# Kernel tuning notes

Measured on AMD Instinct MI355X. Metric: run time of the kernel, lower is better.

Reference implementation:

```python
import jax, jax.numpy as jnp
import numpy as np

HIDDEN = 768
NUM_HEADS = 12
HEAD_SIZE = HIDDEN // NUM_HEADS
LN_EPS = 1e-12


def setup_inputs() -> dict:
    key = jax.random.key(0)
    ks = jax.random.split(key, 10)
    B, S, H = 32, 512, HIDDEN
    std = 1.0 / np.sqrt(H)
    inp = {
        "x": jax.random.normal(ks[0], (B, S, H), dtype=jnp.float32),
        "additive_attention_mask": jnp.zeros((B, 1, 1, S), dtype=jnp.float32),
        "Wq": jax.random.normal(ks[1], (H, H), dtype=jnp.float32) * std,
        "bq": jax.random.normal(ks[2], (H,), dtype=jnp.float32) * 0.02,
        "Wk": jax.random.normal(ks[3], (H, H), dtype=jnp.float32) * std,
        "bk": jax.random.normal(ks[4], (H,), dtype=jnp.float32) * 0.02,
        "Wv": jax.random.normal(ks[5], (H, H), dtype=jnp.float32) * std,
        "bv": jax.random.normal(ks[6], (H,), dtype=jnp.float32) * 0.02,
        "Wo": jax.random.normal(ks[7], (H, H), dtype=jnp.float32) * std,
        "bo": jax.random.normal(ks[8], (H,), dtype=jnp.float32) * 0.02,
        "ln_w": jnp.ones((H,), dtype=jnp.float32),
        "ln_b": jnp.zeros((H,), dtype=jnp.float32),
    }
    return inp


def _split_heads(y):
    # (b, s, h) -> (b, n_heads, s, head_size)
    b, s, _ = y.shape
    return y.reshape(b, s, NUM_HEADS, HEAD_SIZE).transpose(0, 2, 1, 3)


def reference(x, additive_attention_mask, Wq, bq, Wk, bk, Wv, bv, Wo, bo, ln_w, ln_b):
    # Linear projections (torch Linear: x @ W.T + b)
    q = _split_heads(x @ Wq.T + bq)  # b n s d
    k = _split_heads(x @ Wk.T + bk)
    v = _split_heads(x @ Wv.T + bv)

    scores = jnp.einsum("bnqd,bnkd->bnqk", q, k) / np.sqrt(HEAD_SIZE)
    scores = scores + additive_attention_mask  # (b,1,1,s) broadcasts
    attn = jax.nn.softmax(scores, axis=-1)

    weighted = jnp.einsum("bnqk,bnkd->bnqd", attn, v)
    b, n, s, d = weighted.shape
    weighted = weighted.transpose(0, 2, 1, 3).reshape(b, s, n * d)
    attn_out = weighted @ Wo.T + bo

    # residual + LayerNorm (dropout is identity in eval)
    y = x + attn_out
    mean = jnp.mean(y, axis=-1, keepdims=True)
    var = jnp.var(y, axis=-1, keepdims=True)
    y = (y - mean) / jnp.sqrt(var + LN_EPS)
    return y * ln_w + ln_b
```

## Files before the change

### kernel.cpp

```cpp
#include <hip/hip_runtime.h>

#define HIDDEN 768
#define NHEAD 12
#define HDIM 64
#define SEQ 512
#define BATCH 32
#define MTOT (BATCH*SEQ)

typedef __attribute__((ext_vector_type(8))) short short8;
typedef __attribute__((ext_vector_type(4))) float f32x4;
typedef __attribute__((ext_vector_type(4))) unsigned short us4;

#define LOG2E 1.44269504088896340736f

__device__ __forceinline__ unsigned short f2bf(float f){
  unsigned u = __builtin_bit_cast(unsigned, f);
  u += 0x7fff + ((u >> 16) & 1);
  return (unsigned short)(u >> 16);
}

__device__ __forceinline__ float bf2f(unsigned short s){
  unsigned u = ((unsigned)s) << 16;
  return __builtin_bit_cast(float, u);
}

__device__ __forceinline__ float fexp2(float x){
  float r;
  asm("v_exp_f32 %0, %1\n\ts_nop 0" : "=v"(r) : "v"(x));
  return r;
}

__device__ __forceinline__ void gload16(unsigned short* lds, const unsigned short* g){
  __builtin_amdgcn_global_load_lds(
      (const __attribute__((address_space(1))) void*)g,
      (__attribute__((address_space(3))) void*)lds, 16, 0, 0);
}

__global__ __launch_bounds__(256) void cvt_kernel(const float* __restrict__ in,
                                                  unsigned short* __restrict__ out, int n4){
  int i = blockIdx.x * blockDim.x + threadIdx.x;
  if (i >= n4) return;
  float4 v = ((const float4*)in)[i];
  ushort4 o;
  o.x = f2bf(v.x); o.y = f2bf(v.y); o.z = f2bf(v.z); o.w = f2bf(v.w);
  ((ushort4*)out)[i] = o;
}

__global__ __launch_bounds__(256) void cvt4_kernel(
    const float* __restrict__ w0, const float* __restrict__ w1,
    const float* __restrict__ w2, const float* __restrict__ w3,
    unsigned short* __restrict__ o0, unsigned short* __restrict__ o1,
    unsigned short* __restrict__ o2, unsigned short* __restrict__ o3){
  const int which = blockIdx.y;
  const float* in = (which==0)?w0:((which==1)?w1:((which==2)?w2:w3));
  unsigned short* out = (which==0)?o0:((which==1)?o1:((which==2)?o2:o3));
  int i = blockIdx.x * blockDim.x + threadIdx.x;
  float4 v = ((const float4*)in)[i];
  ushort4 o;
  o.x = f2bf(v.x); o.y = f2bf(v.y); o.z = f2bf(v.z); o.w = f2bf(v.w);
  ((ushort4*)out)[i] = o;
}

#define STAGE_A(buf, kt_) do { \
    const int kc_ = (kt_)*64; \
    gload16(&sA[buf][(size_t)(tid)*8],      gA + kc_); \
    gload16(&sA[buf][(size_t)(512+tid)*8],  gA + (size_t)64*HIDDEN + kc_); \
    gload16(&sA[buf][(size_t)(1024+tid)*8], gA + (size_t)128*HIDDEN + kc_); \
    gload16(&sA[buf][(size_t)(1536+tid)*8], gA + (size_t)192*HIDDEN + kc_); \
  } while(0)

#define STAGE_B(buf, kt_) do { \
    const int kc_ = (kt_)*64; \
    gload16(&sB[buf][(size_t)(tid)*8],      gB + kc_); \
    gload16(&sB[buf][(size_t)(512+tid)*8],  gB + (size_t)64*HIDDEN + kc_); \
    gload16(&sB[buf][(size_t)(1024+tid)*8], gB + (size_t)128*HIDDEN + kc_); \
  } while(0)

#define GEMM8_MAIN() \
  STAGE_A(0, 0); STAGE_B(0, 0); \
  for (int kt = 0; kt < 12; ++kt) { \
    const int c = kt & 1; \
    asm volatile("s_waitcnt vmcnt(0)" ::: "memory"); \
    __builtin_amdgcn_s_barrier(); \
    __builtin_amdgcn_sched_barrier(0); \
    const unsigned short* bA = sA[c]; \
    const unsigned short* bB = sB[c]; \
    short8 bf0[3], bf1[3]; \
    _Pragma("unroll") \
    for (int q = 0; q < 4; ++q) { \
      if (kt < 11) { \
        if (q == 0) STAGE_A(c^1, kt+1); \
        else if (q == 1) STAGE_B(c^1, kt+1); \
      } \
      short8 a00 = *(const short8*)&bA[aoff[q*2]]; \
      short8 a01 = *(const short8*)&bA[aoff[q*2] ^ 32]; \
      short8 a10 = *(const short8*)&bA[aoff[q*2+1]]; \
      short8 a11 = *(const short8*)&bA[aoff[q*2+1] ^ 32]; \
      if (q == 0) { \
        _Pragma("unroll") \
        for (int i = 0; i < 3; i++){ \
          bf0[i] = *(const short8*)&bB[boff[i]]; \
          bf1[i] = *(const short8*)&bB[boff[i] ^ 32]; \
        } \
      } \
      asm volatile("s_waitcnt lgkmcnt(0)" ::: "memory"); \
      __builtin_amdgcn_sched_barrier(0); \
      __builtin_amdgcn_s_setprio(1); \
      _Pragma("unroll") \
      for (int ni = 0; ni < 3; ni++){ \
        acc[q*2][ni]   = __builtin_amdgcn_mfma_f32_16x16x32_bf16(a00, bf0[ni], acc[q*2][ni], 0, 0, 0); \
        acc[q*2][ni]   = __builtin_amdgcn_mfma_f32_16x16x32_bf16(a01, bf1[ni], acc[q*2][ni], 0, 0, 0); \
        acc[q*2+1][ni] = __builtin_amdgcn_mfma_f32_16x16x32_bf16(a10, bf0[ni], acc[q*2+1][ni], 0, 0, 0); \
        acc[q*2+1][ni] = __builtin_amdgcn_mfma_f32_16x16x32_bf16(a11, bf1[ni], acc[q*2+1][ni], 0, 0, 0); \
      } \
      __builtin_amdgcn_s_setprio(0); \
      __builtin_amdgcn_sched_barrier(0); \
      __builtin_amdgcn_s_barrier(); \
    } \
  }

__global__ __launch_bounds__(512, 2) void qkv_gemm(
    const unsigned short* __restrict__ A,
    const unsigned short* __restrict__ Wq,
    const unsigned short* __restrict__ Wk,
    const unsigned short* __restrict__ Wv,
    const float* __restrict__ bq,
    const float* __restrict__ bk,
    const float* __restrict__ bv,
    unsigned short* __restrict__ Qo,
    unsigned short* __restrict__ Ko,
    unsigned short* __restrict__ VTo)
{
  __shared__ unsigned short sA[2][16384];
  __shared__ unsigned short sB[2][12288];

  const int flat = blockIdx.x;
  const int swzb = (flat & 7) * 96 + (flat >> 3);
  const int mi_ = swzb / 12;
  const int rem = swzb % 12;
  const int mode = rem >> 2;
  const int n0 = (rem & 3) * 192;
  const int m0 = mi_ * 256;
  const unsigned short* W = (mode==0) ? Wq : ((mode==1) ? Wk : Wv);
  const float* bias = (mode==0) ? bq : ((mode==1) ? bk : bv);

  const int tid = threadIdx.x;
  const int lane = tid & 63;
  const int wid = tid >> 6;
  const int wm = wid >> 2, wn = wid & 3;
  const int g = lane >> 4, l16 = lane & 15;

  const int rS = tid >> 3;
  const int gc = (tid & 7) ^ (rS & 7);
  const unsigned short* gA = &A[(size_t)(m0 + rS)*HIDDEN + gc*8];
  const unsigned short* gB = &W[(size_t)(n0 + rS)*HIDDEN + gc*8];

  int aoff[8], boff[3];
  #pragma unroll
  for (int i = 0; i < 8; i++){
    int rm = wm*128 + i*16 + l16;
    aoff[i] = rm*64 + ((g ^ (rm&7)) * 8);
  }
  #pragma unroll
  for (int i = 0; i < 3; i++){
    int rn = wn*48 + i*16 + l16;
    boff[i] = rn*64 + ((g ^ (rn&7)) * 8);
  }

  f32x4 acc[8][3];
  #pragma unroll
  for (int i = 0; i < 8; i++)
    #pragma unroll
    for (int j = 0; j < 3; j++) acc[i][j] = (f32x4){0.f,0.f,0.f,0.f};

  GEMM8_MAIN();

  float bvv[3];
  #pragma unroll
  for (int ni = 0; ni < 3; ni++) bvv[ni] = bias[n0 + wn*48 + ni*16 + l16];
  #pragma unroll
  for (int mi2 = 0; mi2 < 8; mi2++) {
    int mbase = m0 + wm*128 + mi2*16 + g*4;
    int b = mbase >> 9, s = mbase & 511;
    #pragma unroll
    for (int ni = 0; ni < 3; ni++) {
      int ncol = n0 + wn*48 + ni*16 + l16;
      int h = ncol >> 6, d = ncol & 63;
      if (mode == 2) {
        us4 v;
        #pragma unroll
        for (int r = 0; r < 4; r++) v[r] = f2bf(acc[mi2][ni][r] + bvv[ni]);
        *(us4*)&VTo[(((size_t)(b*NHEAD)+h)*HDIM + d)*SEQ + s] = v;
      } else {
        #pragma unroll
        for (int r = 0; r < 4; r++) {
          float val = acc[mi2][ni][r] + bvv[ni];
          if (mode == 0) Qo[(((size_t)(b*NHEAD)+h)*SEQ + s + r)*HDIM + d] = f2bf(val * 0.1803368801f);
          else           Ko[(((size_t)(b*NHEAD)+h)*SEQ + s + r)*HDIM + d] = f2bf(val);
        }
      }
    }
  }
}

__global__ __launch_bounds__(512, 2) void proj_gemm(
    const unsigned short* __restrict__ A,
    const unsigned short* __restrict__ W,
    const float* __restrict__ bias,
    unsigned short* __restrict__ Out)
{
  __shared__ unsigned short sA[2][16384];
  __shared__ unsigned short sB[2][12288];

  const int flat = blockIdx.x;
  const int swzb = (flat & 7) * 32 + (flat >> 3);
  const int m0 = (swzb >> 2) * 256;
  const int n0 = (swzb & 3) * 192;

  const int tid = threadIdx.x;
  const int lane = tid & 63;
  const int wid = tid >> 6;
  const int wm = wid >> 2, wn = wid & 3;
  const int g = lane >> 4, l16 = lane & 15;

  const int rS = tid >> 3;
  const int gc = (tid & 7) ^ (rS & 7);
  const unsigned short* gA = &A[(size_t)(m0 + rS)*HIDDEN + gc*8];
  const unsigned short* gB = &W[(size_t)(n0 + rS)*HIDDEN + gc*8];

  int aoff[8], boff[3];
  #pragma unroll
  for (int i = 0; i < 8; i++){
    int rm = wm*128 + i*16 + l16;
    aoff[i] = rm*64 + ((g ^ (rm&7)) * 8);
  }
  #pragma unroll
  for (int i = 0; i < 3; i++){
    int rn = wn*48 + i*16 + l16;
    boff[i] = rn*64 + ((g ^ (rn&7)) * 8);
  }

  f32x4 acc[8][3];
  #pragma unroll
  for (int i = 0; i < 8; i++)
    #pragma unroll
    for (int j = 0; j < 3; j++) acc[i][j] = (f32x4){0.f,0.f,0.f,0.f};

  GEMM8_MAIN();

  float bvv[3];
  #pragma unroll
  for (int ni = 0; ni < 3; ni++) bvv[ni] = bias[n0 + wn*48 + ni*16 + l16];
  #pragma unroll
  for (int mi2 = 0; mi2 < 8; mi2++) {
    int mbase = m0 + wm*128 + mi2*16 + g*4;
    #pragma unroll
    for (int ni = 0; ni < 3; ni++) {
      int ncol = n0 + wn*48 + ni*16 + l16;
      #pragma unroll
      for (int r = 0; r < 4; r++)
        Out[(size_t)(mbase + r)*HIDDEN + ncol] = f2bf(acc[mi2][ni][r] + bvv[ni]);
    }
  }
}

__global__ __launch_bounds__(256) void attn_kernel(
    const unsigned short* __restrict__ Q,
    const unsigned short* __restrict__ K,
    const unsigned short* __restrict__ VT,
    const float* __restrict__ mask,
    unsigned short* __restrict__ ctx)
{
  __shared__ unsigned short sK[3][4096];
  __shared__ unsigned short sV[3][4096];
  __shared__ unsigned short P_lds[4*16*68];
  __shared__ float sMask[512];

  const int flat = blockIdx.x;
  const int swzb = (flat & 7) * 192 + (flat >> 3);
  const int qt = swzb & 3;
  const int bh = swzb >> 2;
  const int b = bh / NHEAD, h = bh % NHEAD;
  const int tid = threadIdx.x;
  const int lane = tid & 63;
  const int wid = tid >> 6;
  const int g = lane >> 4, l16 = lane & 15;
  const int qbase = qt*128 + wid*32;

  const int rS = tid >> 3;
  const int cbS = (tid & 7) ^ (rS & 7);
  const size_t khb = (size_t)bh * SEQ;
  const unsigned short* gK  = &K[(khb + rS)*HDIM + cbS*8];
  const unsigned short* gK2 = gK + (size_t)32*HDIM;
  const unsigned short* gV  = &VT[((size_t)bh*HDIM + rS)*SEQ + cbS*8];
  const unsigned short* gV2 = gV + (size_t)32*SEQ;

  sMask[tid]       = mask[b*SEQ + tid] * LOG2E;
  sMask[tid + 256] = mask[b*SEQ + tid + 256] * LOG2E;

  short8 aQ0[2], aQ1[2];
  #pragma unroll
  for (int q16 = 0; q16 < 2; q16++){
    const unsigned short* qp = &Q[(khb + qbase + q16*16 + l16)*HDIM];
    aQ0[q16] = *(const short8*)&qp[g*8];
    aQ1[q16] = *(const short8*)&qp[32 + g*8];
  }

  int off[4];
  {
    const int sw = (g ^ (l16 & 7)) * 8;
    #pragma unroll
    for (int i = 0; i < 4; i++) off[i] = (i*16 + l16)*64 + sw;
  }

  float l_r[2][4];
  f32x4 o_acc[2][4];
  #pragma unroll
  for (int q16 = 0; q16 < 2; q16++){
    #pragma unroll
    for (int r = 0; r < 4; r++) l_r[q16][r] = 0.f;
    #pragma unroll
    for (int dt = 0; dt < 4; dt++) o_acc[q16][dt] = (f32x4){0.f,0.f,0.f,0.f};
  }

#define KSTAGE(buf_, t_) do { \
    gload16(&sK[buf_][wid*512],        gK  + (size_t)(t_)*64*HDIM); \
    gload16(&sK[buf_][2048 + wid*512], gK2 + (size_t)(t_)*64*HDIM); \
    gload16(&sV[buf_][wid*512],        gV  + (t_)*64); \
    gload16(&sV[buf_][2048 + wid*512], gV2 + (t_)*64); \
  } while(0)

  KSTAGE(0, 0);
  KSTAGE(1, 1);
  asm volatile("s_waitcnt lgkmcnt(0)" ::: "memory");

  int cb = 0;
  for (int kt = 0; kt < 8; ++kt) {
    if (kt < 7) asm volatile("s_waitcnt vmcnt(4)" ::: "memory");
    else        asm volatile("s_waitcnt vmcnt(0)" ::: "memory");
    __builtin_amdgcn_s_barrier();
    __builtin_amdgcn_sched_barrier(0);
    if (kt < 6) { const int sb = (cb == 0) ? 2 : cb - 1; KSTAGE(sb, kt + 2); }
    const unsigned short* bK = sK[cb];
    const unsigned short* bV = sV[cb];
    const int kv0 = kt * 64;

    f32x4 sacc[2][4];
    #pragma unroll
    for (int ct = 0; ct < 4; ++ct) {
      short8 k0 = *(const short8*)&bK[off[ct]];
      short8 k1 = *(const short8*)&bK[off[ct] ^ 32];
      f32x4 s0 = (f32x4){0.f,0.f,0.f,0.f}, s1 = (f32x4){0.f,0.f,0.f,0.f};
      __builtin_amdgcn_s_setprio(1);
      s0 = __builtin_amdgcn_mfma_f32_16x16x32_bf16(aQ0[0], k0, s0, 0, 0, 0);
      s0 = __builtin_amdgcn_mfma_f32_16x16x32_bf16(aQ1[0], k1, s0, 0, 0, 0);
      s1 = __builtin_amdgcn_mfma_f32_16x16x32_bf16(aQ0[1], k0, s1, 0, 0, 0);
      s1 = __builtin_amdgcn_mfma_f32_16x16x32_bf16(aQ1[1], k1, s1, 0, 0, 0);
      __builtin_amdgcn_s_setprio(0);
      float mv = sMask[kv0 + ct*16 + l16];
      sacc[0][ct] = s0 + mv;
      sacc[1][ct] = s1 + mv;
    }

    #pragma unroll
    for (int q16 = 0; q16 < 2; q16++){
      #pragma unroll
      for (int ct = 0; ct < 4; ct++){
        #pragma unroll
        for (int r = 0; r < 4; r++){
          float p = fexp2(sacc[q16][ct][r]);
          l_r[q16][r] += p;
          P_lds[(wid*16 + g*4 + r)*68 + ct*16 + l16] =
              (unsigned short)(__builtin_bit_cast(unsigned, p) >> 16);
        }
      }
      asm volatile("s_waitcnt lgkmcnt(0)" ::: "memory");
      __builtin_amdgcn_sched_barrier(0);
      short8 pa0 = *(const short8*)&P_lds[(wid*16 + l16)*68 + g*8];
      short8 pa1 = *(const short8*)&P_lds[(wid*16 + l16)*68 + 32 + g*8];
      __builtin_amdgcn_s_setprio(1);
      #pragma unroll
      for (int dt = 0; dt < 4; dt++){
        short8 v0 = *(const short8*)&bV[off[dt]];
        short8 v1 = *(const short8*)&bV[off[dt] ^ 32];
        o_acc[q16][dt] = __builtin_amdgcn_mfma_f32_16x16x32_bf16(pa0, v0, o_acc[q16][dt], 0, 0, 0);
        o_acc[q16][dt] = __builtin_amdgcn_mfma_f32_16x16x32_bf16(pa1, v1, o_acc[q16][dt], 0, 0, 0);
      }
      __builtin_amdgcn_s_setprio(0);
    }
    cb = (cb == 2) ? 0 : cb + 1;
  }

  #pragma unroll
  for (int q16 = 0; q16 < 2; q16++){
    #pragma unroll
    for (int o = 1; o <= 8; o <<= 1){
      #pragma unroll
      for (int r = 0; r < 4; r++) l_r[q16][r] += __shfl_xor(l_r[q16][r], o);
    }
    float inv[4];
    #pragma unroll
    for (int r = 0; r < 4; r++) inv[r] = 1.f / l_r[q16][r];
    #pragma unroll
    for (int dt = 0; dt < 4; dt++){
      #pragma unroll
      for (int r = 0; r < 4; r++){
        int s = qbase + q16*16 + g*4 + r;
        ctx[((size_t)(b*SEQ + s))*HIDDEN + h*HDIM + dt*16 + l16] = f2bf(o_acc[q16][dt][r] * inv[r]);
      }
    }
  }
#undef KSTAGE
}

__global__ __launch_bounds__(256) void resid_ln(
    const unsigned short* __restrict__ xb, const unsigned short* __restrict__ ao,
    const float* __restrict__ lnw, const float* __restrict__ lnb,
    float* __restrict__ out)
{
  const int row = blockIdx.x*4 + (threadIdx.x >> 6);
  const int lane = threadIdx.x & 63;
  const ushort4* xr = (const ushort4*)&xb[(size_t)row*HIDDEN];
  const ushort4* ar = (const ushort4*)&ao[(size_t)row*HIDDEN];
  float4 y[3];
  float s1 = 0.f, s2 = 0.f;
  #pragma unroll
  for (int j = 0; j < 3; j++){
    ushort4 xv = xr[lane + j*64];
    ushort4 av = ar[lane + j*64];
    float4 v;
    v.x = bf2f(xv.x) + bf2f(av.x); v.y = bf2f(xv.y) + bf2f(av.y);
    v.z = bf2f(xv.z) + bf2f(av.z); v.w = bf2f(xv.w) + bf2f(av.w);
    y[j] = v;
    s1 += v.x + v.y + v.z + v.w;
    s2 += v.x*v.x + v.y*v.y + v.z*v.z + v.w*v.w;
  }
  #pragma unroll
  for (int o = 1; o <= 32; o <<= 1){
    s1 += __shfl_xor(s1, o);
    s2 += __shfl_xor(s2, o);
  }
  float mean = s1 * (1.f/768.f);
  float var = s2 * (1.f/768.f) - mean*mean;
  float rstd = rsqrtf(var + 1e-12f);
  float4* orow = (float4*)&out[(size_t)row*HIDDEN];
  #pragma unroll
  for (int j = 0; j < 3; j++){
    float4 gm = ((const float4*)lnw)[lane + j*64];
    float4 bt = ((const float4*)lnb)[lane + j*64];
    float4 o;
    o.x = (y[j].x - mean)*rstd*gm.x + bt.x;
    o.y = (y[j].y - mean)*rstd*gm.y + bt.y;
    o.z = (y[j].z - mean)*rstd*gm.z + bt.z;
    o.w = (y[j].w - mean)*rstd*gm.w + bt.w;
    orow[lane + j*64] = o;
  }
}

extern "C" void kernel_launch(void* const* d_in, const int* in_sizes, int n_in,
                              void* d_out, int out_size, void* d_ws, size_t ws_size,
                              hipStream_t stream) {
  (void)in_sizes; (void)n_in; (void)out_size; (void)ws_size;
  const float* x    = (const float*)d_in[0];
  const float* mask = (const float*)d_in[1];
  const float* Wq   = (const float*)d_in[2];
  const float* bq   = (const float*)d_in[3];
  const float* Wk   = (const float*)d_in[4];
  const float* bk   = (const float*)d_in[5];
  const float* Wv   = (const float*)d_in[6];
  const float* bv   = (const float*)d_in[7];
  const float* Wo   = (const float*)d_in[8];
  const float* bo   = (const float*)d_in[9];
  const float* lnw  = (const float*)d_in[10];
  const float* lnb  = (const float*)d_in[11];
  float* out = (float*)d_out;

  char* w = (char*)d_ws;
  size_t off = 0;
  auto alloc = [&](size_t bytes) -> char* {
    char* p = w + off; off += (bytes + 255) & ~(size_t)255; return p;
  };
  unsigned short* xb  = (unsigned short*)alloc((size_t)MTOT*HIDDEN*2);
  unsigned short* wqb = (unsigned short*)alloc((size_t)HIDDEN*HIDDEN*2);
  unsigned short* wkb = (unsigned short*)alloc((size_t)HIDDEN*HIDDEN*2);
  unsigned short* wvb = (unsigned short*)alloc((size_t)HIDDEN*HIDDEN*2);
  unsigned short* wob = (unsigned short*)alloc((size_t)HIDDEN*HIDDEN*2);
  unsigned short* qb  = (unsigned short*)alloc((size_t)MTOT*HDIM*NHEAD*2);
  unsigned short* kb  = (unsigned short*)alloc((size_t)MTOT*HDIM*NHEAD*2);
  unsigned short* vtb = (unsigned short*)alloc((size_t)MTOT*HDIM*NHEAD*2);
  unsigned short* ctxb= (unsigned short*)alloc((size_t)MTOT*HIDDEN*2);
  unsigned short* attn_out = qb;

  cvt_kernel<<<dim3(MTOT*HIDDEN/4/256), 256, 0, stream>>>(x, xb, MTOT*HIDDEN/4);
  cvt4_kernel<<<dim3(HIDDEN*HIDDEN/4/256, 4), 256, 0, stream>>>(Wq, Wk, Wv, Wo, wqb, wkb, wvb, wob);

  qkv_gemm<<<dim3(768), 512, 0, stream>>>(xb, wqb, wkb, wvb, bq, bk, bv, qb, kb, vtb);

  attn_kernel<<<dim3(1536), 256, 0, stream>>>(qb, kb, vtb, mask, ctxb);

  proj_gemm<<<dim3(256), 512, 0, stream>>>(ctxb, wob, bo, attn_out);

  resid_ln<<<dim3(MTOT/4), 256, 0, stream>>>(xb, attn_out, lnw, lnb, out);
}
```

Baseline: 194.6 us.

## Simplify GEMM main loop to per-k-half fragment loads with fewer barriers

```diff
diff --git a/kernel.cpp b/kernel.cpp
--- a/kernel.cpp
+++ b/kernel.cpp
@@ -61,6 +61,7 @@
   ((ushort4*)out)[i] = o;
 }
 
+
 #define STAGE_A(buf, kt_) do { \
     const int kc_ = (kt_)*64; \
     gload16(&sA[buf][(size_t)(tid)*8],      gA + kc_); \
@@ -76,46 +77,31 @@
     gload16(&sB[buf][(size_t)(1024+tid)*8], gB + (size_t)128*HIDDEN + kc_); \
   } while(0)
 
-#define GEMM8_MAIN() \
+#define GEMM_MAIN() \
   STAGE_A(0, 0); STAGE_B(0, 0); \
   for (int kt = 0; kt < 12; ++kt) { \
     const int c = kt & 1; \
     asm volatile("s_waitcnt vmcnt(0)" ::: "memory"); \
     __builtin_amdgcn_s_barrier(); \
-    __builtin_amdgcn_sched_barrier(0); \
+    if (kt < 11) { STAGE_A(c^1, kt+1); STAGE_B(c^1, kt+1); } \
     const unsigned short* bA = sA[c]; \
     const unsigned short* bB = sB[c]; \
-    short8 bf0[3], bf1[3]; \
     _Pragma("unroll") \
-    for (int q = 0; q < 4; ++q) { \
-      if (kt < 11) { \
-        if (q == 0) STAGE_A(c^1, kt+1); \
-        else if (q == 1) STAGE_B(c^1, kt+1); \
-      } \
-      short8 a00 = *(const short8*)&bA[aoff[q*2]]; \
-      short8 a01 = *(const short8*)&bA[aoff[q*2] ^ 32]; \
-      short8 a10 = *(const short8*)&bA[aoff[q*2+1]]; \
-      short8 a11 = *(const short8*)&bA[aoff[q*2+1] ^ 32]; \
-      if (q == 0) { \
-        _Pragma("unroll") \
-        for (int i = 0; i < 3; i++){ \
-          bf0[i] = *(const short8*)&bB[boff[i]]; \
-          bf1[i] = *(const short8*)&bB[boff[i] ^ 32]; \
-        } \
-      } \
+    for (int kk = 0; kk < 2; ++kk) { \
+      short8 af[8], bf[3]; \
+      _Pragma("unroll") \
+      for (int i = 0; i < 8; i++) af[i] = *(const short8*)&bA[aoff[i] ^ (kk*32)]; \
+      _Pragma("unroll") \
+      for (int i = 0; i < 3; i++) bf[i] = *(const short8*)&bB[boff[i] ^ (kk*32)]; \
       asm volatile("s_waitcnt lgkmcnt(0)" ::: "memory"); \
       __builtin_amdgcn_sched_barrier(0); \
       __builtin_amdgcn_s_setprio(1); \
       _Pragma("unroll") \
-      for (int ni = 0; ni < 3; ni++){ \
-        acc[q*2][ni]   = __builtin_amdgcn_mfma_f32_16x16x32_bf16(a00, bf0[ni], acc[q*2][ni], 0, 0, 0); \
-        acc[q*2][ni]   = __builtin_amdgcn_mfma_f32_16x16x32_bf16(a01, bf1[ni], acc[q*2][ni], 0, 0, 0); \
-        acc[q*2+1][ni] = __builtin_amdgcn_mfma_f32_16x16x32_bf16(a10, bf0[ni], acc[q*2+1][ni], 0, 0, 0); \
-        acc[q*2+1][ni] = __builtin_amdgcn_mfma_f32_16x16x32_bf16(a11, bf1[ni], acc[q*2+1][ni], 0, 0, 0); \
-      } \
+      for (int mi2 = 0; mi2 < 8; mi2++) \
+        _Pragma("unroll") \
+        for (int ni = 0; ni < 3; ni++) \
+          acc[mi2][ni] = __builtin_amdgcn_mfma_f32_16x16x32_bf16(af[mi2], bf[ni], acc[mi2][ni], 0, 0, 0); \
       __builtin_amdgcn_s_setprio(0); \
-      __builtin_amdgcn_sched_barrier(0); \
-      __builtin_amdgcn_s_barrier(); \
     } \
   }
 
@@ -173,7 +159,7 @@
     #pragma unroll
     for (int j = 0; j < 3; j++) acc[i][j] = (f32x4){0.f,0.f,0.f,0.f};
 
-  GEMM8_MAIN();
+  GEMM_MAIN();
 
   float bvv[3];
   #pragma unroll
@@ -246,7 +232,7 @@
     #pragma unroll
     for (int j = 0; j < 3; j++) acc[i][j] = (f32x4){0.f,0.f,0.f,0.f};
 
-  GEMM8_MAIN();
+  GEMM_MAIN();
 
   float bvv[3];
   #pragma unroll
```

After: 192.7 us. Within noise of the previous version (-1.0%).
